# Kernel tuning notes

Measured on AMD Instinct MI355X. Metric: run time of the kernel, lower is better.

The kernel has to match this reference:

```python
import jax, jax.numpy as jnp
import numpy as np

SURROGATE_SCALE = 10.0  # SuperSpike-style surrogate slope

@jax.custom_vjp
def spike_fn(v):
    # Heaviside forward (standard SNN spike function)
    return (v > 0).astype(v.dtype)

def _spike_fwd(v):
    return spike_fn(v), v

def _spike_bwd(v, g):
    surrogate = 1.0 / (SURROGATE_SCALE * jnp.abs(v) + 1.0) ** 2
    return (g * surrogate,)

spike_fn.defvjp(_spike_fwd, _spike_bwd)

def setup_inputs() -> dict:
    key = jax.random.key(0)
    B, C, T = 128, 512, 1024
    x = jax.random.normal(key, (B, C, T), dtype=jnp.float32)
    beta = jnp.asarray(0.65, dtype=jnp.float32)   # scalar leak (non-trainable default)
    Vth = jnp.ones((C,), dtype=jnp.float32)        # threshold per channel
    return {"x": x, "beta": beta, "Vth": Vth}

def reference(x, beta, Vth):
    # x: (B, C, T)  -- time_position=2, negative_mempot=True, flatten_output=False
    B, C, T = x.shape
    xs = jnp.moveaxis(x, 2, 0)  # (T, B, C): scan over time

    def step(carry, inp):
        mem, spk = carry
        rst = spk * Vth                 # einsum('ab,b->ab', spk, Vth)
        mem = mem * beta + inp - rst    # negative_mempot branch
        spk = spike_fn(mem - Vth)
        return (mem, spk), spk

    init = (jnp.zeros((B, C), x.dtype), jnp.zeros((B, C), x.dtype))
    _, spk_rec = jax.lax.scan(step, init, xs)   # (T, B, C)
    return jnp.moveaxis(spk_rec, 0, 2)          # (B, C, T)
```

## Files before the change

### kernel.cpp

```cpp
#include <hip/hip_runtime.h>


#define LIF_BC 65536
#define LIF_T  1024
#define CHUNK  256
#define NP     (LIF_T / CHUNK)
#define ROWS   16
#define JPT    ROWS

using fvec4 = __attribute__((ext_vector_type(4))) float;

__global__ __launch_bounds__(64) void lif_fwd(
    const float* __restrict__ x,
    const float* __restrict__ beta_p,
    const float* __restrict__ vth_p,
    float* __restrict__ out)
{
    __shared__ float lds[ROWS * CHUNK];

    const int lane = threadIdx.x;
    const int r0   = blockIdx.x * ROWS;

    const float beta = beta_p[0];
    const float vth  = vth_p[(r0 + lane) & 511];

    fvec4 pf[JPT];

    auto issue_loads = [&](int ph) {
#pragma unroll
        for (int j = 0; j < JPT; ++j) {
            pf[j] = __builtin_nontemporal_load(
                (const fvec4*)&x[(size_t)(r0 + j) * LIF_T
                                 + (size_t)ph * CHUNK + lane * 4]);
        }
    };

    auto write_lds = [&]() {
#pragma unroll
        for (int j = 0; j < JPT; ++j) {
            const int slot = lane ^ j;
            *(fvec4*)&lds[j * CHUNK + slot * 4] = pf[j];
        }
    };

    float mem = 0.0f, spk = 0.0f;

    auto compute = [&]() {
        if (lane < ROWS) {
            const int rbase = lane * CHUNK;
            const int sw    = lane;
#pragma unroll
            for (int g = 0; g < CHUNK / 4; ++g) {
                const int slot = g ^ sw;
                fvec4 v = *(fvec4*)&lds[rbase + slot * 4];
#pragma unroll
                for (int e = 0; e < 4; ++e) {
                    float rst = __fmul_rn(spk, vth);
                    mem = __fsub_rn(__fadd_rn(__fmul_rn(mem, beta), v[e]), rst);
                    spk = (__fsub_rn(mem, vth) > 0.0f) ? 1.0f : 0.0f;
                    v[e] = spk;
                }
                *(fvec4*)&lds[rbase + slot * 4] = v;
            }
        }
    };

    auto store_tile = [&](int ph) {
#pragma unroll
        for (int j = 0; j < JPT; ++j) {
            const int slot = lane ^ j;
            fvec4 s = *(const fvec4*)&lds[j * CHUNK + slot * 4];
            __builtin_nontemporal_store(
                s, (fvec4*)&out[(size_t)(r0 + j) * LIF_T
                                + (size_t)ph * CHUNK + lane * 4]);
        }
    };

    issue_loads(0);
    write_lds();
    issue_loads(1);

    for (int k = 0; k < NP; ++k) {
        compute();
        store_tile(k);
        if (k + 1 < NP) write_lds();
        if (k + 2 < NP) issue_loads(k + 2);
    }
}

extern "C" void kernel_launch(void* const* d_in, const int* in_sizes, int n_in,
                              void* d_out, int out_size, void* d_ws, size_t ws_size,
                              hipStream_t stream) {
    const float* x    = (const float*)d_in[0];
    const float* beta = (const float*)d_in[1];
    const float* vth  = (const float*)d_in[2];
    float* out = (float*)d_out;

    dim3 grid(LIF_BC / ROWS);
    lif_fwd<<<grid, 64, 0, stream>>>(x, beta, vth, out);
}
```

Baseline: 466.6 us.

## Double-buffer LDS tiles with smaller chunks and two-row-per-wave loads

```diff
diff --git a/kernel.cpp b/kernel.cpp
--- a/kernel.cpp
+++ b/kernel.cpp
@@ -3,10 +3,10 @@
 
 #define LIF_BC 65536
 #define LIF_T  1024
-#define CHUNK  256
+#define CHUNK  128
 #define NP     (LIF_T / CHUNK)
 #define ROWS   16
-#define JPT    ROWS
+#define JPT    8
 
 using fvec4 = __attribute__((ext_vector_type(4))) float;
 
@@ -16,7 +16,8 @@
     const float* __restrict__ vth_p,
     float* __restrict__ out)
 {
-    __shared__ float lds[ROWS * CHUNK];
+    __shared__ float ldsA[ROWS * CHUNK];
+    __shared__ float ldsB[ROWS * CHUNK];
 
     const int lane = threadIdx.x;
     const int r0   = blockIdx.x * ROWS;
@@ -24,67 +25,78 @@
     const float beta = beta_p[0];
     const float vth  = vth_p[(r0 + lane) & 511];
 
+    const int l_row2 = lane >> 5;
+    const int l_t    = lane & 31;
+
     fvec4 pf[JPT];
 
     auto issue_loads = [&](int ph) {
 #pragma unroll
         for (int j = 0; j < JPT; ++j) {
+            const int row = 2 * j + l_row2;
             pf[j] = __builtin_nontemporal_load(
-                (const fvec4*)&x[(size_t)(r0 + j) * LIF_T
-                                 + (size_t)ph * CHUNK + lane * 4]);
+                (const fvec4*)&x[(size_t)(r0 + row) * LIF_T
+                                 + (size_t)ph * CHUNK + l_t * 4]);
         }
     };
 
-    auto write_lds = [&]() {
+    auto write_lds = [&](float* buf) {
 #pragma unroll
         for (int j = 0; j < JPT; ++j) {
-            const int slot = lane ^ j;
-            *(fvec4*)&lds[j * CHUNK + slot * 4] = pf[j];
+            const int row  = 2 * j + l_row2;
+            const int slot = l_t ^ (row & 15);
+            *(fvec4*)&buf[row * CHUNK + slot * 4] = pf[j];
         }
     };
 
-    float mem = 0.0f, spk = 0.0f;
+    float mem = 0.0f, rst = 0.0f;
 
-    auto compute = [&]() {
+    auto compute = [&](float* buf) {
         if (lane < ROWS) {
             const int rbase = lane * CHUNK;
-            const int sw    = lane;
+            const int sw    = lane & 15;
 #pragma unroll
             for (int g = 0; g < CHUNK / 4; ++g) {
                 const int slot = g ^ sw;
-                fvec4 v = *(fvec4*)&lds[rbase + slot * 4];
+                fvec4 v = *(fvec4*)&buf[rbase + slot * 4];
 #pragma unroll
                 for (int e = 0; e < 4; ++e) {
-                    float rst = __fmul_rn(spk, vth);
-                    mem = __fsub_rn(__fadd_rn(__fmul_rn(mem, beta), v[e]), rst);
-                    spk = (__fsub_rn(mem, vth) > 0.0f) ? 1.0f : 0.0f;
-                    v[e] = spk;
+                    float a = __fadd_rn(__fmul_rn(mem, beta), v[e]);
+                    mem = __fsub_rn(a, rst);
+                    const bool s = __fsub_rn(mem, vth) > 0.0f;
+                    rst  = s ? vth : 0.0f;
+                    v[e] = s ? 1.0f : 0.0f;
                 }
-                *(fvec4*)&lds[rbase + slot * 4] = v;
+                *(fvec4*)&buf[rbase + slot * 4] = v;
             }
         }
     };
 
-    auto store_tile = [&](int ph) {
+    auto store_tile = [&](const float* buf, int ph) {
 #pragma unroll
         for (int j = 0; j < JPT; ++j) {
-            const int slot = lane ^ j;
-            fvec4 s = *(const fvec4*)&lds[j * CHUNK + slot * 4];
+            const int row  = 2 * j + l_row2;
+            const int slot = l_t ^ (row & 15);
+            fvec4 s = *(const fvec4*)&buf[row * CHUNK + slot * 4];
             __builtin_nontemporal_store(
-                s, (fvec4*)&out[(size_t)(r0 + j) * LIF_T
-                                + (size_t)ph * CHUNK + lane * 4]);
+                s, (fvec4*)&out[(size_t)(r0 + row) * LIF_T
+                                + (size_t)ph * CHUNK + l_t * 4]);
         }
     };
 
     issue_loads(0);
-    write_lds();
+    write_lds(ldsA);
     issue_loads(1);
 
-    for (int k = 0; k < NP; ++k) {
-        compute();
-        store_tile(k);
-        if (k + 1 < NP) write_lds();
+    for (int k = 0; k < NP; k += 2) {
+        compute(ldsA);
+        write_lds(ldsB);
         if (k + 2 < NP) issue_loads(k + 2);
+        store_tile(ldsA, k);
+        compute(ldsB);
+        if (k + 2 < NP) write_lds(ldsA);
+        if (k + 3 < NP) issue_loads(k + 3);
+        store_tile(ldsB, k + 1);
     }
 }
 
```

After: 447.8 us. -4.0%, faster.
